# Performance work log

Hardware: AMD Instinct MI355X
Metric: run time of the kernel (lower is better)

The kernel has to match this reference:

```python
import jax, jax.numpy as jnp
import numpy as np

OUT_H, OUT_W, GRID_SIZE = 256, 192, 5
N = GRID_SIZE * GRID_SIZE
BATCH = 64


def _make_constants():
    ax = np.linspace(-1.0, 1.0, GRID_SIZE)
    P_Y, P_X = np.meshgrid(ax, ax)
    P_X = P_X.reshape(-1).astype(np.float64)  # (N,)
    P_Y = P_Y.reshape(-1).astype(np.float64)
    d2 = (P_X[:, None] - P_X[None, :]) ** 2 + (P_Y[:, None] - P_Y[None, :]) ** 2
    d2[d2 == 0] = 1.0
    K = d2 * np.log(d2)
    P = np.stack([np.ones(N), P_X, P_Y], axis=1)  # (N,3)
    L = np.block([[K, P], [P.T, np.zeros((3, 3))]])  # (N+3, N+3)
    Li = np.linalg.inv(L).astype(np.float32)
    grid_X, grid_Y = np.meshgrid(np.linspace(-1, 1, OUT_W), np.linspace(-1, 1, OUT_H))
    return (P_X.astype(np.float32), P_Y.astype(np.float32), Li,
            grid_X.astype(np.float32), grid_Y.astype(np.float32))


_PX, _PY, _LI, _GX, _GY = _make_constants()


def setup_inputs() -> dict:
    key = jax.random.key(0)
    theta = jax.random.normal(key, (BATCH, 2 * N), dtype=jnp.float32) * 0.1
    return {"theta": theta}


def reference(theta) -> jnp.ndarray:
    P_X = jnp.asarray(_PX)          # (N,)
    P_Y = jnp.asarray(_PY)
    Li = jnp.asarray(_LI)           # (N+3, N+3)
    grid_X = jnp.asarray(_GX)       # (H, W)
    grid_Y = jnp.asarray(_GY)

    # Absolute control-point targets
    Q_X = theta[:, :N] + P_X        # (B, N)
    Q_Y = theta[:, N:] + P_Y

    # TPS coefficients: non-affine W (B,N) and affine A (B,3)
    W_X = jnp.einsum('nm,bm->bn', Li[:N, :N], Q_X)
    W_Y = jnp.einsum('nm,bm->bn', Li[:N, :N], Q_Y)
    A_X = jnp.einsum('km,bm->bk', Li[N:, :N], Q_X)  # (B,3): [c, cx, cy]
    A_Y = jnp.einsum('km,bm->bk', Li[N:, :N], Q_Y)

    # RBF kernel U(r^2) = r^2 log(r^2), evaluated per pixel per control point
    d2 = (grid_X[:, :, None] - P_X) ** 2 + (grid_Y[:, :, None] - P_Y) ** 2  # (H,W,N)
    d2 = jnp.where(d2 == 0, jnp.float32(1.0), d2)
    U = d2 * jnp.log(d2)            # (H,W,N)

    rbf_X = jnp.einsum('hwn,bn->bhw', U, W_X)
    rbf_Y = jnp.einsum('hwn,bn->bhw', U, W_Y)

    px = (A_X[:, 0, None, None] + A_X[:, 1, None, None] * grid_X
          + A_X[:, 2, None, None] * grid_Y + rbf_X)  # (B,H,W)
    py = (A_Y[:, 0, None, None] + A_Y[:, 1, None, None] * grid_X
          + A_Y[:, 2, None, None] * grid_Y + rbf_Y)

    return jnp.stack([px, py], axis=3)  # (B,H,W,2)
```

## Files before the change

kernel.cpp:

```cpp
#include <hip/hip_runtime.h>

#define OUT_H 256
#define OUT_W 192
#define HWPIX (OUT_H * OUT_W)
#define BATCH 64

typedef float v2f __attribute__((ext_vector_type(2)));


constexpr double cx_ln(double x) {
  int e = 0;
  while (x >= 1.5) { x *= 0.5; ++e; }
  while (x < 0.75) { x *= 2.0; --e; }
  double t = (x - 1.0) / (x + 1.0);
  double t2 = t * t, s = 0.0, term = t;
  for (int k = 0; k < 20; ++k) { s += term / (double)(2 * k + 1); term *= t2; }
  return 2.0 * s + (double)e * 0.6931471805599453094172321214581766;
}

struct Consts {
  float li[28][25];
  float cp[2][28];
};

constexpr Consts make_consts() {
  Consts out{};
  double PX[25] = {}, PY[25] = {};
  for (int n = 0; n < 25; ++n) {
    PX[n] = -1.0 + 0.5 * (double)(n / 5);
    PY[n] = -1.0 + 0.5 * (double)(n % 5);
  }
  double M[28][56] = {};
  for (int i = 0; i < 28; ++i)
    for (int j = 0; j < 56; ++j) M[i][j] = 0.0;
  for (int i = 0; i < 25; ++i) {
    for (int j = 0; j < 25; ++j) {
      double dx = PX[i] - PX[j], dy = PY[i] - PY[j];
      double d2 = dx * dx + dy * dy;
      M[i][j] = (d2 == 0.0) ? 0.0 : d2 * cx_ln(d2);
    }
    M[i][25] = 1.0; M[i][26] = PX[i]; M[i][27] = PY[i];
    M[25][i] = 1.0; M[26][i] = PX[i]; M[27][i] = PY[i];
  }
  for (int i = 0; i < 28; ++i) M[i][28 + i] = 1.0;
  for (int k = 0; k < 28; ++k) {
    int piv = k;
    double mx = M[k][k] < 0.0 ? -M[k][k] : M[k][k];
    for (int r = k + 1; r < 28; ++r) {
      double a = M[r][k] < 0.0 ? -M[r][k] : M[r][k];
      if (a > mx) { mx = a; piv = r; }
    }
    if (piv != k)
      for (int j = 0; j < 56; ++j) { double t = M[k][j]; M[k][j] = M[piv][j]; M[piv][j] = t; }
    double inv = 1.0 / M[k][k];
    for (int j = 0; j < 56; ++j) M[k][j] *= inv;
    for (int r = 0; r < 28; ++r) {
      if (r == k) continue;
      double f = M[r][k];
      if (f != 0.0)
        for (int j = 0; j < 56; ++j) M[r][j] -= f * M[k][j];
    }
  }
  for (int k = 0; k < 28; ++k)
    for (int m = 0; m < 25; ++m) out.li[k][m] = (float)M[k][28 + m];
  for (int axis = 0; axis < 2; ++axis)
    for (int k = 0; k < 28; ++k) {
      double s = 0.0;
      for (int m = 0; m < 25; ++m)
        s += (double)out.li[k][m] * (axis ? PY[m] : PX[m]);
      out.cp[axis][k] = (float)s;
    }
  return out;
}

constexpr Consts CC = make_consts();

__device__ constexpr float PXf[25] = {
  -1.f,-1.f,-1.f,-1.f,-1.f, -0.5f,-0.5f,-0.5f,-0.5f,-0.5f,
   0.f, 0.f, 0.f, 0.f, 0.f,  0.5f, 0.5f, 0.5f, 0.5f, 0.5f,
   1.f, 1.f, 1.f, 1.f, 1.f };
__device__ constexpr float PYf[25] = {
  -1.f,-0.5f,0.f,0.5f,1.f, -1.f,-0.5f,0.f,0.5f,1.f,
  -1.f,-0.5f,0.f,0.5f,1.f, -1.f,-0.5f,0.f,0.5f,1.f,
  -1.f,-0.5f,0.f,0.5f,1.f };


__global__ __launch_bounds__(256) void tps_fused(const float* __restrict__ theta,
                                                 v2f* __restrict__ out) {
  __shared__ float sth[BATCH * 50];
  __shared__ float sC[BATCH * 56];
  const int t = threadIdx.x;

  {
    const float4* g4 = (const float4*)theta;
    float4* s4 = (float4*)sth;
#pragma unroll
    for (int i = 0; i < 4; ++i) {
      int idx = t + i * 256;
      if (idx < 800) s4[idx] = g4[idx];
    }
  }
  __syncthreads();

  {
    const int pair = t & 127;
    const int b = pair >> 1, axis = pair & 1;
    const int kg = t >> 7;
    float th[25];
    const float* src = sth + b * 50 + axis * 25;
#pragma unroll
    for (int m = 0; m < 25; ++m) th[m] = src[m];
#pragma unroll
    for (int j = 0; j < 14; ++j) {
      const int k = kg * 14 + j;
      float acc = CC.cp[axis][k];
#pragma unroll
      for (int m = 0; m < 25; ++m) acc += CC.li[k][m] * th[m];
      sC[b * 56 + k * 2 + axis] = acc;
    }
  }
  __syncthreads();

  const int lane = t & 63;
  const int wg = t >> 6;
  const int p = (blockIdx.x << 6) + lane;
  const int w = p % OUT_W;
  const int h = p / OUT_W;
  float gx = (float)(-1.0 + (double)w * (2.0 / 191.0));
  float gy = (float)(-1.0 + (double)h * (2.0 / 255.0));
  if (w == OUT_W - 1) gx = 1.0f;
  if (h == OUT_H - 1) gy = 1.0f;

  float U[28];
#pragma unroll
  for (int n = 0; n < 25; ++n) {
    float dx = gx - PXf[n];
    float dy = gy - PYf[n];
    float d2 = dx * dx + dy * dy;
    float u = d2 * __logf(d2);
    U[n] = (d2 == 0.0f) ? 0.0f : u;
  }
  U[25] = 1.0f; U[26] = gx; U[27] = gy;

  const float4* cb = (const float4*)sC + wg * 16 * 14;
  v2f* op = out + p;
#pragma unroll 4
  for (int i = 0; i < 16; ++i) {
    const float4* c4 = cb + i * 14;
    v2f acc = {0.f, 0.f};
#pragma unroll
    for (int j = 0; j < 14; ++j) {
      float4 c = c4[j];
      v2f c01 = {c.x, c.y};
      v2f c23 = {c.z, c.w};
      v2f u0 = {U[2 * j], U[2 * j]};
      v2f u1 = {U[2 * j + 1], U[2 * j + 1]};
      acc = __builtin_elementwise_fma(u0, c01, acc);
      acc = __builtin_elementwise_fma(u1, c23, acc);
    }
    const int b = wg * 16 + i;
    __builtin_nontemporal_store(acc, op + b * HWPIX);
  }
}


extern "C" void kernel_launch(void* const* d_in, const int* in_sizes, int n_in,
                              void* d_out, int out_size, void* d_ws, size_t ws_size,
                              hipStream_t stream) {
  const float* theta = (const float*)d_in[0];
  v2f* out = (v2f*)d_out;
  hipLaunchKernelGGL(tps_fused, dim3(HWPIX / 64), dim3(256), 0, stream, theta, out);
}
```

Before: 73.25 us.

## Process two pixels per thread and split batch across block pairs

```diff
diff --git a/kernel.cpp b/kernel.cpp
--- a/kernel.cpp
+++ b/kernel.cpp
@@ -6,6 +6,7 @@
 #define BATCH 64
 
 typedef float v2f __attribute__((ext_vector_type(2)));
+typedef float v4f __attribute__((ext_vector_type(4)));
 
 
 constexpr double cx_ln(double x) {
@@ -86,33 +87,35 @@
 
 
 __global__ __launch_bounds__(256) void tps_fused(const float* __restrict__ theta,
-                                                 v2f* __restrict__ out) {
-  __shared__ float sth[BATCH * 50];
-  __shared__ float sC[BATCH * 56];
+                                                 v4f* __restrict__ out4) {
+  __shared__ float sth[32 * 50];
+  __shared__ float sC[32 * 56];
   const int t = threadIdx.x;
+  const int pg = blockIdx.x >> 1;
+  const int bg = blockIdx.x & 1;
 
   {
-    const float4* g4 = (const float4*)theta;
+    const float4* g4 = (const float4*)theta + bg * 400;
     float4* s4 = (float4*)sth;
 #pragma unroll
-    for (int i = 0; i < 4; ++i) {
+    for (int i = 0; i < 2; ++i) {
       int idx = t + i * 256;
-      if (idx < 800) s4[idx] = g4[idx];
+      if (idx < 400) s4[idx] = g4[idx];
     }
   }
   __syncthreads();
 
   {
-    const int pair = t & 127;
+    const int pair = t & 63;
     const int b = pair >> 1, axis = pair & 1;
-    const int kg = t >> 7;
+    const int kg = t >> 6;
     float th[25];
     const float* src = sth + b * 50 + axis * 25;
 #pragma unroll
     for (int m = 0; m < 25; ++m) th[m] = src[m];
 #pragma unroll
-    for (int j = 0; j < 14; ++j) {
-      const int k = kg * 14 + j;
+    for (int j = 0; j < 7; ++j) {
+      const int k = kg * 7 + j;
       float acc = CC.cp[axis][k];
 #pragma unroll
       for (int m = 0; m < 25; ++m) acc += CC.li[k][m] * th[m];
@@ -122,44 +125,55 @@
   __syncthreads();
 
   const int lane = t & 63;
-  const int wg = t >> 6;
-  const int p = (blockIdx.x << 6) + lane;
-  const int w = p % OUT_W;
-  const int h = p / OUT_W;
-  float gx = (float)(-1.0 + (double)w * (2.0 / 191.0));
-  float gy = (float)(-1.0 + (double)h * (2.0 / 255.0));
-  if (w == OUT_W - 1) gx = 1.0f;
+  const int wv = t >> 6;
+  const int p0 = pg * 128 + lane * 2;
+  const int w0 = p0 % OUT_W;
+  const int h = p0 / OUT_W;
+  float gx0 = (float)(-1.0 + (double)w0 * (2.0 / 191.0));
+  float gx1 = (float)(-1.0 + (double)(w0 + 1) * (2.0 / 191.0));
+  float gy  = (float)(-1.0 + (double)h * (2.0 / 255.0));
+  if (w0 + 1 == OUT_W - 1) gx1 = 1.0f;
   if (h == OUT_H - 1) gy = 1.0f;
 
-  float U[28];
+  float U0[28], U1[28];
 #pragma unroll
   for (int n = 0; n < 25; ++n) {
-    float dx = gx - PXf[n];
-    float dy = gy - PYf[n];
-    float d2 = dx * dx + dy * dy;
-    float u = d2 * __logf(d2);
-    U[n] = (d2 == 0.0f) ? 0.0f : u;
+    float dyv = gy - PYf[n];
+    float dy2 = dyv * dyv;
+    float dx0 = gx0 - PXf[n];
+    float dx1 = gx1 - PXf[n];
+    float d20 = dx0 * dx0 + dy2;
+    float d21 = dx1 * dx1 + dy2;
+    float u0 = d20 * __logf(d20);
+    float u1 = d21 * __logf(d21);
+    U0[n] = (d20 == 0.0f) ? 0.0f : u0;
+    U1[n] = (d21 == 0.0f) ? 0.0f : u1;
   }
-  U[25] = 1.0f; U[26] = gx; U[27] = gy;
+  U0[25] = 1.0f; U0[26] = gx0; U0[27] = gy;
+  U1[25] = 1.0f; U1[26] = gx1; U1[27] = gy;
 
-  const float4* cb = (const float4*)sC + wg * 16 * 14;
-  v2f* op = out + p;
-#pragma unroll 4
-  for (int i = 0; i < 16; ++i) {
+  const float4* cb = (const float4*)sC + wv * 8 * 14;
+  v4f* op = out4 + (size_t)(bg * 32 + wv * 8) * (HWPIX / 2) + (pg * 64 + lane);
+#pragma unroll 2
+  for (int i = 0; i < 8; ++i) {
     const float4* c4 = cb + i * 14;
-    v2f acc = {0.f, 0.f};
+    v2f a0 = {0.f, 0.f}, a1 = {0.f, 0.f};
 #pragma unroll
     for (int j = 0; j < 14; ++j) {
       float4 c = c4[j];
       v2f c01 = {c.x, c.y};
       v2f c23 = {c.z, c.w};
-      v2f u0 = {U[2 * j], U[2 * j]};
-      v2f u1 = {U[2 * j + 1], U[2 * j + 1]};
-      acc = __builtin_elementwise_fma(u0, c01, acc);
-      acc = __builtin_elementwise_fma(u1, c23, acc);
+      v2f u00 = {U0[2 * j], U0[2 * j]};
+      v2f u01 = {U0[2 * j + 1], U0[2 * j + 1]};
+      v2f u10 = {U1[2 * j], U1[2 * j]};
+      v2f u11 = {U1[2 * j + 1], U1[2 * j + 1]};
+      a0 = __builtin_elementwise_fma(u00, c01, a0);
+      a0 = __builtin_elementwise_fma(u01, c23, a0);
+      a1 = __builtin_elementwise_fma(u10, c01, a1);
+      a1 = __builtin_elementwise_fma(u11, c23, a1);
     }
-    const int b = wg * 16 + i;
-    __builtin_nontemporal_store(acc, op + b * HWPIX);
+    v4f res = {a0.x, a0.y, a1.x, a1.y};
+    __builtin_nontemporal_store(res, op + (size_t)i * (HWPIX / 2));
   }
 }
 
@@ -168,6 +182,6 @@
                               void* d_out, int out_size, void* d_ws, size_t ws_size,
                               hipStream_t stream) {
   const float* theta = (const float*)d_in[0];
-  v2f* out = (v2f*)d_out;
-  hipLaunchKernelGGL(tps_fused, dim3(HWPIX / 64), dim3(256), 0, stream, theta, out);
+  v4f* out4 = (v4f*)d_out;
+  hipLaunchKernelGGL(tps_fused, dim3(768), dim3(256), 0, stream, theta, out4);
 }
```

Result: faster. 71.55 us (-2.3%).
